# Kernel optimization log

Hardware: AMD Instinct MI355X
Metric: run time of the kernel (lower is better)

The kernel has to match this reference:

```python
import jax, jax.numpy as jnp
import numpy as np

LENGTH = 512
Q = 2 * LENGTH + 3  # num_states = 2*length + 3
ALPHA = 26          # amino-acid alphabet size
BATCH = 256
T = 512


def setup_inputs() -> dict:
    key = jax.random.key(0)
    k1, k2, k3, k4 = jax.random.split(key, 4)
    x = jax.random.randint(k1, (BATCH, T), 0, ALPHA, dtype=jnp.int32)
    A_logits = jax.random.normal(k2, (Q, Q), dtype=jnp.float32)
    B_logits = jax.random.normal(k3, (Q, ALPHA), dtype=jnp.float32)
    init_logits = jax.random.normal(k4, (Q,), dtype=jnp.float32)
    return {"x": x, "A_logits": A_logits, "B_logits": B_logits, "init_logits": init_logits}


def reference(x, A_logits, B_logits, init_logits):
    # Build stochastic matrices (as emitter/transitioner do from their kernels).
    A = jax.nn.softmax(A_logits, axis=-1)        # (q, q) row-stochastic transitions
    B = jax.nn.softmax(B_logits, axis=-1)        # (q, alpha) emission distributions
    init = jax.nn.softmax(init_logits)           # (q,) initial distribution

    # Precompute per-position emission probs: E[b, t, :] = B[:, x[b, t]]
    E = B.T[x]                                   # (B, T, q)

    # First step (self.init branch): forward = E0 * initial distribution
    f0 = E[:, 0] * init[None, :]                 # (B, q)
    S0 = jnp.sum(f0, axis=-1, keepdims=True)     # (B, 1)
    ll0 = jnp.log(S0)
    f0 = f0 / S0

    def step(carry, Et):
        f, ll = carry
        fwd = Et * (f @ A)                       # emit * transition  (B, q)
        S = jnp.sum(fwd, axis=-1, keepdims=True)
        ll = ll + jnp.log(S)
        fwd = fwd / S
        return (fwd, ll), fwd

    (_, loglik), fwd_seq = jax.lax.scan(step, (f0, ll0), jnp.swapaxes(E[:, 1:], 0, 1))
    # fwd_seq: (T-1, B, q) -> full (B, T, q) with first step prepended
    forward = jnp.swapaxes(jnp.concatenate([f0[None], fwd_seq], axis=0), 0, 1)
    return forward, loglik
```

## Files before the change

kernel.cpp:

```cpp
#include <hip/hip_runtime.h>
#include <stdint.h>


#define Q     1027
#define TT    512
#define ALPH  26
#define KCH   33
#define NTILE 65
#define NCHK  (KCH*64)
#define GIMG  (NCHK*16)
#define NCL   16
#define WPC   16
#define MB    16

typedef short  short8  __attribute__((ext_vector_type(8)));
typedef float  floatx4 __attribute__((ext_vector_type(4)));
typedef int    intx4   __attribute__((ext_vector_type(4)));

static constexpr size_t al512(size_t x) { return (x + 511) & ~size_t(511); }
static constexpr size_t OFF_APACK = 0;
static constexpr size_t SZ_APACK  = (size_t)NTILE * KCH * 64 * 16;
static constexpr size_t OFF_BSOFT = al512(OFF_APACK + SZ_APACK);
static constexpr size_t SZ_BSOFT  = (size_t)Q * ALPH * 4;
static constexpr size_t OFF_INIT  = al512(OFF_BSOFT + SZ_BSOFT);
static constexpr size_t OFF_AMAX  = al512(OFF_INIT + Q * 4);
static constexpr size_t OFF_AINV  = al512(OFF_AMAX + Q * 4);
static constexpr size_t OFF_GEX   = al512(OFF_AINV + Q * 4);
static constexpr size_t SZ_GEX    = (size_t)NCL * 2 * GIMG;
static constexpr size_t OFF_SP    = al512(OFF_GEX + SZ_GEX);
static constexpr size_t SZ_SP     = (size_t)NCL * 2 * 64 * MB * 4;
static constexpr size_t OFF_FLAGS = al512(OFF_SP + SZ_SP);
static constexpr size_t SZ_FLAGS  = (size_t)NCL * 64 * 4;
static constexpr size_t WS_NEED   = OFF_FLAGS + SZ_FLAGS;
static constexpr size_t FWDSZ     = (size_t)256 * TT * Q;

__device__ __forceinline__ uint32_t f2bf(float f) {
  uint32_t u = __float_as_uint(f);
  return (u + 0x7fffu + ((u >> 16) & 1u)) >> 16;
}


__global__ void k_zero(char* __restrict__ ws) {
  const size_t n = (WS_NEED - OFF_GEX) / 16;
  intx4* p = (intx4*)(ws + OFF_GEX);
  for (size_t i = (size_t)blockIdx.x * 256 + threadIdx.x; i < n; i += (size_t)80 * 256)
    p[i] = intx4{0, 0, 0, 0};
}

__global__ void k_astats(const float* __restrict__ A, char* __restrict__ ws) {
  const int r = blockIdx.x, tid = threadIdx.x;
  const float* row = A + (size_t)r * Q;
  __shared__ float red[4], red2[4];
  float mx = -3.0e38f;
  for (int i = tid; i < Q; i += 256) mx = fmaxf(mx, row[i]);
#pragma unroll
  for (int d = 1; d < 64; d <<= 1) mx = fmaxf(mx, __shfl_xor(mx, d));
  if ((tid & 63) == 0) red[tid >> 6] = mx;
  __syncthreads();
  mx = fmaxf(fmaxf(red[0], red[1]), fmaxf(red[2], red[3]));
  float s = 0.f;
  for (int i = tid; i < Q; i += 256) s += expf(row[i] - mx);
#pragma unroll
  for (int d = 1; d < 64; d <<= 1) s += __shfl_xor(s, d);
  if ((tid & 63) == 0) red2[tid >> 6] = s;
  __syncthreads();
  s = red2[0] + red2[1] + red2[2] + red2[3];
  if (tid == 0) {
    *(float*)(ws + OFF_AMAX + (size_t)r * 4) = mx;
    *(float*)(ws + OFF_AINV + (size_t)r * 4) = 1.0f / s;
  }
}

__global__ void k_bsoft(const float* __restrict__ Bl, char* __restrict__ ws) {
  const int r = blockIdx.x, l = threadIdx.x;
  float v = (l < ALPH) ? Bl[(size_t)r * ALPH + l] : -3.0e38f;
  float mx = v;
#pragma unroll
  for (int d = 1; d < 64; d <<= 1) mx = fmaxf(mx, __shfl_xor(mx, d));
  float e = (l < ALPH) ? expf(v - mx) : 0.f;
  float s = e;
#pragma unroll
  for (int d = 1; d < 64; d <<= 1) s += __shfl_xor(s, d);
  if (l < ALPH) *(float*)(ws + OFF_BSOFT + ((size_t)r * ALPH + l) * 4) = e / s;
}

__global__ void k_isoft(const float* __restrict__ il, char* __restrict__ ws) {
  const int tid = threadIdx.x;
  __shared__ float red[4], red2[4];
  float mx = -3.0e38f;
  for (int i = tid; i < Q; i += 256) mx = fmaxf(mx, il[i]);
#pragma unroll
  for (int d = 1; d < 64; d <<= 1) mx = fmaxf(mx, __shfl_xor(mx, d));
  if ((tid & 63) == 0) red[tid >> 6] = mx;
  __syncthreads();
  mx = fmaxf(fmaxf(red[0], red[1]), fmaxf(red[2], red[3]));
  float s = 0.f;
  for (int i = tid; i < Q; i += 256) s += expf(il[i] - mx);
#pragma unroll
  for (int d = 1; d < 64; d <<= 1) s += __shfl_xor(s, d);
  if ((tid & 63) == 0) red2[tid >> 6] = s;
  __syncthreads();
  s = red2[0] + red2[1] + red2[2] + red2[3];
  const float inv = 1.0f / s;
  for (int i = tid; i < Q; i += 256)
    *(float*)(ws + OFF_INIT + (size_t)i * 4) = expf(il[i] - mx) * inv;
}

__global__ void k_repack(const float* __restrict__ A, char* __restrict__ ws) {
  const int b = blockIdx.x;
  const int nt = b % NTILE, kc = b / NTILE;
  const int lane = threadIdx.x;
  const int q = nt * 16 + (lane & 15);
  const int kb = kc * 32 + (lane >> 4) * 8;
  union { short8 v; unsigned short u[8]; } pk;
#pragma unroll
  for (int e = 0; e < 8; ++e) {
    const int k = kb + e;
    float val = 0.f;
    if (k < Q && q < Q) {
      const float mxk = *(const float*)(ws + OFF_AMAX + (size_t)k * 4);
      const float ivk = *(const float*)(ws + OFF_AINV + (size_t)k * 4);
      val = expf(A[(size_t)k * Q + q] - mxk) * ivk;
    }
    pk.u[e] = (unsigned short)f2bf(val);
  }
  *(short8*)(ws + OFF_APACK + (((size_t)nt * KCH + kc) * 64 + lane) * 16) = pk.v;
}


__global__ __launch_bounds__(256, 1) void k_main(const int* __restrict__ xin,
                                                 char* __restrict__ ws,
                                                 float* __restrict__ out) {
  const int bid = blockIdx.x;
  const int c = bid & 15, j = bid >> 4;
  const int tid = threadIdx.x;
  const int lane = tid & 63, w = tid >> 6;
  const int cL = lane & 15, g4 = lane >> 4;
  const int tg = 4 * j + w;
  const bool jx = (j == 15), two = (jx && w == 3);
  const uint64_t wsu = (uint64_t)(uintptr_t)ws;

  __shared__ floatx4 accx[4][5][64];
  __shared__ uint8_t x_lds[MB * TT];
  __shared__ float   B_lds[5][16][ALPH];
  __shared__ float   init_lds[5][16];
  __shared__ float   SpW[4][16];

  for (int idx = tid; idx < MB * TT; idx += 256)
    x_lds[idx] = (uint8_t)xin[(size_t)(c * MB) * TT + idx];
  for (int idx = tid; idx < 5 * 16 * ALPH; idx += 256) {
    const int tl = idx / (16 * ALPH), rem = idx % (16 * ALPH);
    const int cc = rem / ALPH, a = rem % ALPH;
    const int grow = (tl < 4 ? 64 * j + tl * 16 : 1024) + cc;
    B_lds[tl][cc][a] = (grow < Q) ? *(const float*)(ws + OFF_BSOFT + ((size_t)grow * ALPH + a) * 4) : 0.f;
  }
  for (int idx = tid; idx < 5 * 16; idx += 256) {
    const int tl = idx / 16, cc = idx % 16;
    const int grow = (tl < 4 ? 64 * j + tl * 16 : 1024) + cc;
    init_lds[tl][cc] = (grow < Q) ? *(const float*)(ws + OFF_INIT + (size_t)grow * 4) : 0.f;
  }

  short8 af[4][9];
#pragma unroll
  for (int tt = 0; tt < 4; ++tt)
#pragma unroll
    for (int i = 0; i < 9; ++i)
      if (i < 8 || w == 0)
        af[tt][i] = *(const short8*)(ws + OFF_APACK +
                      (((size_t)(4 * j + tt) * KCH + (4 * i + w)) * 64 + lane) * 16);
  short8 afx[9];
  if (jx) {
#pragma unroll
    for (int i = 0; i < 9; ++i)
      if (i < 8 || w == 0)
        afx[i] = *(const short8*)(ws + OFF_APACK +
                      (((size_t)64 * KCH + (4 * i + w)) * 64 + lane) * 16);
  }
  __syncthreads();

  float up0[4], upx[4] = {0.f, 0.f, 0.f, 0.f};
  float uold[4], uxold[4] = {0.f, 0.f, 0.f, 0.f};
  float llacc = 0.f;

#define POST_STEP(TCUR)                                                                   \
  do {                                                                                    \
    const int par_ = (TCUR) & 1;                                                          \
    const uint64_t gb_ = wsu + OFF_GEX + (size_t)(c * 2 + par_) * GIMG;                   \
    const uint64_t b0_ = gb_ + (size_t)((tg >> 1) * 1024 + ((tg & 1) * 2 + (cL >> 3)) * 256 \
                         + g4 * 64 + (cL & 7) * 2);                                       \
    float t0_ = up0[0], t1_ = up0[1], t2_ = up0[2], t3_ = up0[3];                         \
    _Pragma("unroll") for (int r = 0; r < 4; ++r) {                                       \
      uint32_t v0_ = f2bf(up0[r]);                                                        \
      asm volatile("global_store_short %0, %1, off sc0 sc1" ::                            \
                   "v"(b0_ + (size_t)(r * 16)), "v"(v0_) : "memory");                     \
    }                                                                                     \
    if (two) {                                                                            \
      const uint64_t bx_ = gb_ + (size_t)(32 * 1024 + (cL >> 3) * 256 + g4 * 64 +         \
                           (cL & 7) * 2);                                                 \
      _Pragma("unroll") for (int r = 0; r < 4; ++r) {                                     \
        uint32_t v1_ = f2bf(upx[r]);                                                      \
        asm volatile("global_store_short %0, %1, off sc0 sc1" ::                          \
                     "v"(bx_ + (size_t)(r * 16)), "v"(v1_) : "memory");                   \
      }                                                                                   \
      t0_ += upx[0]; t1_ += upx[1]; t2_ += upx[2]; t3_ += upx[3];                         \
    }                                                                                     \
    _Pragma("unroll") for (int d = 1; d < 16; d <<= 1) {                                  \
      t0_ += __shfl_xor(t0_, d); t1_ += __shfl_xor(t1_, d);                               \
      t2_ += __shfl_xor(t2_, d); t3_ += __shfl_xor(t3_, d);                               \
    }                                                                                     \
    if (cL == 0) {                                                                        \
      floatx4 sv_; sv_[0] = t0_; sv_[1] = t1_; sv_[2] = t2_; sv_[3] = t3_;                \
      uint64_t sa_ = wsu + OFF_SP + (size_t)(c * 2 + par_) * 4096 +                       \
                     (size_t)(tg * 64 + g4 * 16);                                         \
      asm volatile("global_store_dwordx4 %0, %1, off sc0 sc1" :: "v"(sa_), "v"(sv_)       \
                   : "memory");                                                           \
    }                                                                                     \
    asm volatile("s_waitcnt vmcnt(0)" ::: "memory");                                      \
    __builtin_amdgcn_sched_barrier(0);                                                    \
    if (lane == 0) {                                                                      \
      int fv_ = (TCUR) + 1;                                                               \
      asm volatile("global_store_dword %0, %1, off sc0 sc1" ::                            \
                   "v"(wsu + OFF_FLAGS + (size_t)(c * 64 + tg) * 4), "v"(fv_) : "memory");\
    }                                                                                     \
  } while (0)

#define WAIT_FLAGS(TGT)                                                                   \
  do {                                                                                    \
    if (w == 0) {                                                                         \
      const uint64_t fa_ = wsu + OFF_FLAGS + (size_t)(c * 64 + lane) * 4;                 \
      for (;;) {                                                                          \
        int f_;                                                                           \
        asm volatile("global_load_dword %0, %1, off sc0 sc1\n\ts_waitcnt vmcnt(0)"        \
                     : "=v"(f_) : "v"(fa_) : "memory");                                   \
        if (__all(f_ >= (TGT))) break;                                                    \
        __builtin_amdgcn_s_sleep(2);                                                      \
      }                                                                                   \
    }                                                                                     \
    __syncthreads();                                                                      \
  } while (0)

#pragma unroll
  for (int r = 0; r < 4; ++r) {
    const int m = g4 * 4 + r;
    const int xm = x_lds[m * TT + 0];
    up0[r] = B_lds[w][cL][xm] * init_lds[w][cL];
    uold[r] = up0[r];
    if (two) { upx[r] = B_lds[4][cL][xm] * init_lds[4][cL]; uxold[r] = upx[r]; }
  }
  POST_STEP(0);

  for (int t = 1; t < TT; ++t) {
    const int parp = (t - 1) & 1;
    WAIT_FLAGS(t);

    const uint64_t gb = wsu + OFF_GEX + (size_t)(c * 2 + parp) * GIMG;
    intx4 sg[9], spi;
#pragma unroll
    for (int i = 0; i < 8; ++i)
      asm volatile("global_load_dwordx4 %0, %1, off sc0 sc1"
                   : "=v"(sg[i]) : "v"(gb + (size_t)((i * 256 + tid) * 16)) : "memory");
    if (w == 0)
      asm volatile("global_load_dwordx4 %0, %1, off sc0 sc1"
                   : "=v"(sg[8]) : "v"(gb + (size_t)((2048 + lane) * 16)) : "memory");
    asm volatile("global_load_dwordx4 %0, %1, off sc0 sc1"
                 : "=v"(spi)
                 : "v"(wsu + OFF_SP + (size_t)(c * 2 + parp) * 4096 + (size_t)tid * 16)
                 : "memory");
    asm volatile("s_waitcnt vmcnt(1)" ::: "memory");
    __builtin_amdgcn_sched_barrier(0);

    floatx4 acc[4] = {{0,0,0,0},{0,0,0,0},{0,0,0,0},{0,0,0,0}};
    floatx4 acx = {0, 0, 0, 0};
#pragma unroll
    for (int i = 0; i < 8; ++i) {
      const short8 gf = __builtin_bit_cast(short8, sg[i]);
#pragma unroll
      for (int tt = 0; tt < 4; ++tt)
        acc[tt] = __builtin_amdgcn_mfma_f32_16x16x32_bf16(gf, af[tt][i], acc[tt], 0, 0, 0);
      if (jx) acx = __builtin_amdgcn_mfma_f32_16x16x32_bf16(gf, afx[i], acx, 0, 0, 0);
    }
    if (w == 0) {
      const short8 gf = __builtin_bit_cast(short8, sg[8]);
#pragma unroll
      for (int tt = 0; tt < 4; ++tt)
        acc[tt] = __builtin_amdgcn_mfma_f32_16x16x32_bf16(gf, af[tt][8], acc[tt], 0, 0, 0);
      if (jx) acx = __builtin_amdgcn_mfma_f32_16x16x32_bf16(gf, afx[8], acx, 0, 0, 0);
    }
#pragma unroll
    for (int tt = 0; tt < 4; ++tt) accx[w][tt][lane] = acc[tt];
    if (jx) accx[w][4][lane] = acx;

    asm volatile("s_waitcnt vmcnt(0)" ::: "memory");
    __builtin_amdgcn_sched_barrier(0);
    floatx4 s4 = __builtin_bit_cast(floatx4, spi);
#pragma unroll
    for (int d = 4; d < 64; d <<= 1) {
#pragma unroll
      for (int e = 0; e < 4; ++e) s4[e] += __shfl_xor(s4[e], d);
    }
    if (lane < 4) *(floatx4*)&SpW[w][lane * 4] = s4;
    __syncthreads();

    float invS[4], ot0[4], ot1[4];
    floatx4 rs = accx[0][w][lane] + accx[1][w][lane] + accx[2][w][lane] + accx[3][w][lane];
    float rx[4];
    if (two) {
      floatx4 q = accx[0][4][lane] + accx[1][4][lane] + accx[2][4][lane] + accx[3][4][lane];
#pragma unroll
      for (int r = 0; r < 4; ++r) rx[r] = q[r];
    }
#pragma unroll
    for (int r = 0; r < 4; ++r) {
      const int m = g4 * 4 + r;
      invS[r] = 1.0f / (SpW[0][m] + SpW[1][m] + SpW[2][m] + SpW[3][m]);
      ot0[r] = uold[r] * invS[r];
      if (two) ot1[r] = uxold[r] * invS[r];
      const int xm = x_lds[m * TT + t];
      up0[r] = rs[r] * B_lds[w][cL][xm] * invS[r];
      uold[r] = up0[r];
      if (two) { upx[r] = rx[r] * B_lds[4][cL][xm] * invS[r]; uxold[r] = upx[r]; }
    }

    POST_STEP(t);

#pragma unroll
    for (int r = 0; r < 4; ++r) {
      const int m = g4 * 4 + r;
      const size_t ob = ((size_t)(c * MB + m) * TT + (t - 1)) * Q;
      __builtin_nontemporal_store(ot0[r], out + ob + tg * 16 + cL);
      if (two && cL < 3)
        __builtin_nontemporal_store(ot1[r], out + ob + 1024 + cL);
    }
    if (j == 0 && w == 0 && lane < 16)
      llacc += logf(SpW[0][lane] + SpW[1][lane] + SpW[2][lane] + SpW[3][lane]);
  }

  WAIT_FLAGS(TT);
  {
    const int parp = (TT - 1) & 1;
    intx4 spi;
    asm volatile("global_load_dwordx4 %0, %1, off sc0 sc1\n\ts_waitcnt vmcnt(0)"
                 : "=v"(spi)
                 : "v"(wsu + OFF_SP + (size_t)(c * 2 + parp) * 4096 + (size_t)tid * 16)
                 : "memory");
    __builtin_amdgcn_sched_barrier(0);
    floatx4 s4 = __builtin_bit_cast(floatx4, spi);
#pragma unroll
    for (int d = 4; d < 64; d <<= 1) {
#pragma unroll
      for (int e = 0; e < 4; ++e) s4[e] += __shfl_xor(s4[e], d);
    }
    if (lane < 4) *(floatx4*)&SpW[w][lane * 4] = s4;
    __syncthreads();
    float invS[4];
#pragma unroll
    for (int r = 0; r < 4; ++r) {
      const int m = g4 * 4 + r;
      invS[r] = 1.0f / (SpW[0][m] + SpW[1][m] + SpW[2][m] + SpW[3][m]);
    }
#pragma unroll
    for (int r = 0; r < 4; ++r) {
      const int m = g4 * 4 + r;
      const size_t ob = ((size_t)(c * MB + m) * TT + (TT - 1)) * Q;
      __builtin_nontemporal_store(up0[r] * invS[r], out + ob + tg * 16 + cL);
      if (two && cL < 3)
        __builtin_nontemporal_store(upx[r] * invS[r], out + ob + 1024 + cL);
    }
    if (j == 0 && w == 0 && lane < 16) {
      llacc += logf(SpW[0][lane] + SpW[1][lane] + SpW[2][lane] + SpW[3][lane]);
      out[FWDSZ + (size_t)c * MB + lane] = llacc;
    }
  }
}


extern "C" void kernel_launch(void* const* d_in, const int* in_sizes, int n_in,
                              void* d_out, int out_size, void* d_ws, size_t ws_size,
                              hipStream_t stream) {
  const int*   x    = (const int*)d_in[0];
  const float* Alog = (const float*)d_in[1];
  const float* Blog = (const float*)d_in[2];
  const float* ilog = (const float*)d_in[3];
  char*  ws  = (char*)d_ws;
  float* out = (float*)d_out;
  if (ws_size < WS_NEED) return;

  hipLaunchKernelGGL(k_zero,   dim3(80),          dim3(256), 0, stream, ws);
  hipLaunchKernelGGL(k_astats, dim3(Q),           dim3(256), 0, stream, Alog, ws);
  hipLaunchKernelGGL(k_bsoft,  dim3(Q),           dim3(64),  0, stream, Blog, ws);
  hipLaunchKernelGGL(k_isoft,  dim3(1),           dim3(256), 0, stream, ilog, ws);
  hipLaunchKernelGGL(k_repack, dim3(NTILE * KCH), dim3(64),  0, stream, Alog, ws);
  hipLaunchKernelGGL(k_main,   dim3(NCL * WPC),   dim3(256), 0, stream, x, ws, out);
}
```

Before: 2.152 ms.

## Coalesce bf16 exchange stores via LDS transpose and prefetch flag poll

Each wave now transposes its four per-row forward values through a small LDS buffer, so the bf16 exchange image is written with one packed dwordx2 store per lane instead of four scattered short stores. After publishing its step flag, wave 0 issues the flag poll load early, and the next wait first consumes that prefetched value. This takes one global round-trip off the inter-block barrier critical path. The log-likelihood sum is read from shared memory earlier as well. The changes add LDS traffic and waitcnt barriers, and they rely on the vmcnt accounting staying correct.

```diff
diff --git a/kernel.cpp b/kernel.cpp
--- a/kernel.cpp
+++ b/kernel.cpp
@@ -16,6 +16,7 @@
 typedef short  short8  __attribute__((ext_vector_type(8)));
 typedef float  floatx4 __attribute__((ext_vector_type(4)));
 typedef int    intx4   __attribute__((ext_vector_type(4)));
+typedef int    intx2   __attribute__((ext_vector_type(2)));
 
 static constexpr size_t al512(size_t x) { return (x + 511) & ~size_t(511); }
 static constexpr size_t OFF_APACK = 0;
@@ -145,6 +146,7 @@
   __shared__ float   B_lds[5][16][ALPH];
   __shared__ float   init_lds[5][16];
   __shared__ float   SpW[4][16];
+  __shared__ __attribute__((aligned(16))) float tr_lds[4][16][20];
 
   for (int idx = tid; idx < MB * TT; idx += 256)
     x_lds[idx] = (uint8_t)xin[(size_t)(c * MB) * TT + idx];
@@ -181,29 +183,43 @@
   float up0[4], upx[4] = {0.f, 0.f, 0.f, 0.f};
   float uold[4], uxold[4] = {0.f, 0.f, 0.f, 0.f};
   float llacc = 0.f;
+  int fpre = 0;
+  const uint64_t fapoll = wsu + OFF_FLAGS + (size_t)(c * 64 + lane) * 4;
 
 #define POST_STEP(TCUR)                                                                   \
   do {                                                                                    \
     const int par_ = (TCUR) & 1;                                                          \
     const uint64_t gb_ = wsu + OFF_GEX + (size_t)(c * 2 + par_) * GIMG;                   \
-    const uint64_t b0_ = gb_ + (size_t)((tg >> 1) * 1024 + ((tg & 1) * 2 + (cL >> 3)) * 256 \
-                         + g4 * 64 + (cL & 7) * 2);                                       \
+                                             \
+    _Pragma("unroll") for (int r_ = 0; r_ < 4; ++r_)                                      \
+      tr_lds[w][g4 * 4 + r_][cL] = up0[r_];                                               \
+    asm volatile("s_waitcnt lgkmcnt(0)" ::: "memory");                                    \
+    __builtin_amdgcn_sched_barrier(0);                                                    \
+    {                                                                                     \
+      const floatx4 tv_ = *(const floatx4*)&tr_lds[w][(lane >> 1) & 15]                   \
+                                                   [(lane >> 5) * 8 + (lane & 1) * 4];    \
+      intx2 gv_;                                                                          \
+      gv_[0] = (int)(f2bf(tv_[0]) | (f2bf(tv_[1]) << 16));                                \
+      gv_[1] = (int)(f2bf(tv_[2]) | (f2bf(tv_[3]) << 16));                                \
+      asm volatile("global_store_dwordx2 %0, %1, off sc0 sc1" ::                          \
+                   "v"(gb_ + (size_t)((tg >> 1) * 1024 + (tg & 1) * 512 + lane * 8)),     \
+                   "v"(gv_) : "memory");                                                  \
+    }                                                                                     \
+    if (two) {                                                                            \
+      _Pragma("unroll") for (int r_ = 0; r_ < 4; ++r_)                                    \
+        tr_lds[w][g4 * 4 + r_][cL] = upx[r_];                                             \
+      asm volatile("s_waitcnt lgkmcnt(0)" ::: "memory");                                  \
+      __builtin_amdgcn_sched_barrier(0);                                                  \
+      const floatx4 tx_ = *(const floatx4*)&tr_lds[w][(lane >> 1) & 15]                   \
+                                                   [(lane >> 5) * 8 + (lane & 1) * 4];    \
+      intx2 gx_;                                                                          \
+      gx_[0] = (int)(f2bf(tx_[0]) | (f2bf(tx_[1]) << 16));                                \
+      gx_[1] = (int)(f2bf(tx_[2]) | (f2bf(tx_[3]) << 16));                                \
+      asm volatile("global_store_dwordx2 %0, %1, off sc0 sc1" ::                          \
+                   "v"(gb_ + (size_t)(32 * 1024 + lane * 8)), "v"(gx_) : "memory");       \
+    }                                                                                     \
     float t0_ = up0[0], t1_ = up0[1], t2_ = up0[2], t3_ = up0[3];                         \
-    _Pragma("unroll") for (int r = 0; r < 4; ++r) {                                       \
-      uint32_t v0_ = f2bf(up0[r]);                                                        \
-      asm volatile("global_store_short %0, %1, off sc0 sc1" ::                            \
-                   "v"(b0_ + (size_t)(r * 16)), "v"(v0_) : "memory");                     \
-    }                                                                                     \
-    if (two) {                                                                            \
-      const uint64_t bx_ = gb_ + (size_t)(32 * 1024 + (cL >> 3) * 256 + g4 * 64 +         \
-                           (cL & 7) * 2);                                                 \
-      _Pragma("unroll") for (int r = 0; r < 4; ++r) {                                     \
-        uint32_t v1_ = f2bf(upx[r]);                                                      \
-        asm volatile("global_store_short %0, %1, off sc0 sc1" ::                          \
-                     "v"(bx_ + (size_t)(r * 16)), "v"(v1_) : "memory");                   \
-      }                                                                                   \
-      t0_ += upx[0]; t1_ += upx[1]; t2_ += upx[2]; t3_ += upx[3];                         \
-    }                                                                                     \
+    if (two) { t0_ += upx[0]; t1_ += upx[1]; t2_ += upx[2]; t3_ += upx[3]; }              \
     _Pragma("unroll") for (int d = 1; d < 16; d <<= 1) {                                  \
       t0_ += __shfl_xor(t0_, d); t1_ += __shfl_xor(t1_, d);                               \
       t2_ += __shfl_xor(t2_, d); t3_ += __shfl_xor(t3_, d);                               \
@@ -222,18 +238,21 @@
       asm volatile("global_store_dword %0, %1, off sc0 sc1" ::                            \
                    "v"(wsu + OFF_FLAGS + (size_t)(c * 64 + tg) * 4), "v"(fv_) : "memory");\
     }                                                                                     \
+    if (w == 0)                                                                           \
+      asm volatile("global_load_dword %0, %1, off sc0 sc1"                                \
+                   : "=v"(fpre) : "v"(fapoll) : "memory");                                \
   } while (0)
 
-#define WAIT_FLAGS(TGT)                                                                   \
+#define WAIT_FLAGS(TGT, NCNT)                                                             \
   do {                                                                                    \
     if (w == 0) {                                                                         \
-      const uint64_t fa_ = wsu + OFF_FLAGS + (size_t)(c * 64 + lane) * 4;                 \
-      for (;;) {                                                                          \
-        int f_;                                                                           \
+      asm volatile("s_waitcnt vmcnt(" #NCNT ")" ::: "memory");                            \
+      __builtin_amdgcn_sched_barrier(0);                                                  \
+      int f_ = fpre;                                                                      \
+      while (!__all(f_ >= (TGT))) {                                                       \
+        __builtin_amdgcn_s_sleep(2);                                                      \
         asm volatile("global_load_dword %0, %1, off sc0 sc1\n\ts_waitcnt vmcnt(0)"        \
-                     : "=v"(f_) : "v"(fa_) : "memory");                                   \
-        if (__all(f_ >= (TGT))) break;                                                    \
-        __builtin_amdgcn_s_sleep(2);                                                      \
+                     : "=v"(f_) : "v"(fapoll) : "memory");                                \
       }                                                                                   \
     }                                                                                     \
     __syncthreads();                                                                      \
@@ -251,7 +270,8 @@
 
   for (int t = 1; t < TT; ++t) {
     const int parp = (t - 1) & 1;
-    WAIT_FLAGS(t);
+    if (t == 1) WAIT_FLAGS(t, 0);
+    else        WAIT_FLAGS(t, 4);
 
     const uint64_t gb = wsu + OFF_GEX + (size_t)(c * 2 + parp) * GIMG;
     intx4 sg[9], spi;
@@ -309,6 +329,8 @@
 #pragma unroll
       for (int r = 0; r < 4; ++r) rx[r] = q[r];
     }
+    float llS = 1.f;
+    if (lane < 16) llS = SpW[0][lane] + SpW[1][lane] + SpW[2][lane] + SpW[3][lane];
 #pragma unroll
     for (int r = 0; r < 4; ++r) {
       const int m = g4 * 4 + r;
@@ -331,11 +353,10 @@
       if (two && cL < 3)
         __builtin_nontemporal_store(ot1[r], out + ob + 1024 + cL);
     }
-    if (j == 0 && w == 0 && lane < 16)
-      llacc += logf(SpW[0][lane] + SpW[1][lane] + SpW[2][lane] + SpW[3][lane]);
-  }
-
-  WAIT_FLAGS(TT);
+    if (j == 0 && w == 0 && lane < 16) llacc += logf(llS);
+  }
+
+  WAIT_FLAGS(TT, 4);
   {
     const int parp = (TT - 1) & 1;
     intx4 spi;
@@ -353,6 +374,8 @@
     if (lane < 4) *(floatx4*)&SpW[w][lane * 4] = s4;
     __syncthreads();
     float invS[4];
+    float llS = 1.f;
+    if (lane < 16) llS = SpW[0][lane] + SpW[1][lane] + SpW[2][lane] + SpW[3][lane];
 #pragma unroll
     for (int r = 0; r < 4; ++r) {
       const int m = g4 * 4 + r;
@@ -367,7 +390,7 @@
         __builtin_nontemporal_store(upx[r] * invS[r], out + ob + 1024 + cL);
     }
     if (j == 0 && w == 0 && lane < 16) {
-      llacc += logf(SpW[0][lane] + SpW[1][lane] + SpW[2][lane] + SpW[3][lane]);
+      llacc += logf(llS);
       out[FWDSZ + (size_t)c * MB + lane] = llacc;
     }
   }
```

New measurement: 3.223 ms. 1.5x slower.
